# Kernel optimization log

Measured on AMD Instinct MI355X. Metric: run time of the kernel, lower is better.

## Reference

```python
import jax, jax.numpy as jnp
import numpy as np

VOCAB, EDIM, WFEAT, LABELS, SLOPE = 50000, 128, 128, 2, 0.01
N = 8192

def setup_inputs() -> dict:
    key = jax.random.key(0)
    ks = jax.random.split(key, 8)
    inSen = jax.random.randint(ks[0], (N,), 0, VOCAB, dtype=jnp.int64) if jax.config.read('jax_enable_x64') else jax.random.randint(ks[0], (N,), 0, VOCAB, dtype=jnp.int32)
    adj = jax.random.randint(ks[1], (N, N), 0, 2, dtype=jnp.int32)
    emb = jax.random.normal(ks[2], (VOCAB, EDIM), dtype=jnp.float32)
    W = jax.random.normal(ks[3], (EDIM, WFEAT), dtype=jnp.float32) * (1.0 / np.sqrt(EDIM))
    a_src = jax.random.normal(ks[4], (WFEAT,), dtype=jnp.float32) * (1.0 / np.sqrt(WFEAT))
    a_dst = jax.random.normal(ks[5], (WFEAT,), dtype=jnp.float32) * (1.0 / np.sqrt(WFEAT))
    cls_W = jax.random.normal(ks[6], (WFEAT, LABELS), dtype=jnp.float32) * (1.0 / np.sqrt(WFEAT))
    cls_b = jax.random.normal(ks[7], (LABELS,), dtype=jnp.float32) * 0.01
    return {"inSen": inSen, "adj": adj, "selfLink": 1, "emb": emb, "W": W,
            "a_src": a_src, "a_dst": a_dst, "cls_W": cls_W, "cls_b": cls_b}

def reference(inSen, adj, selfLink, emb, W, a_src, a_dst, cls_W, cls_b):
    # Embedding lookup: (N, edim)
    words = emb[inSen]
    # GAT layer: linear projection then adjacency-masked additive attention
    h = words @ W                              # (N, wFeat)
    f_src = h @ a_src                          # (N,)
    f_dst = h @ a_dst                          # (N,)
    e = jax.nn.leaky_relu(f_src[:, None] + f_dst[None, :], negative_slope=SLOPE)  # (N, N)
    mask = (adj + selfLink * jnp.eye(adj.shape[0], dtype=adj.dtype)) > 0
    e = jnp.where(mask, e, jnp.float32(-1e9))
    attention = jax.nn.softmax(e, axis=1)      # (N, N)
    sentence = attention @ h                   # (N, wFeat)
    # Max pool over words, classify
    poolSentence = jnp.max(sentence, axis=0)   # (wFeat,)
    label = jax.nn.softmax(poolSentence @ cls_W + cls_b, axis=0)  # (labels,)
    return (poolSentence, attention, sentence, label)
```

## Files before the change

### kernel.cpp

```cpp
#include <hip/hip_runtime.h>
#include <hip/hip_bf16.h>

#define NR 8192
#define WF 128
#define MSTRIDE 260

typedef short bf16x8 __attribute__((ext_vector_type(8)));
typedef float f32x4 __attribute__((ext_vector_type(4)));
typedef int   i32x4 __attribute__((ext_vector_type(4)));

static __device__ __forceinline__ unsigned int f2bf(float f) {
    unsigned int u = __float_as_uint(f);
    return (u + 0x7fffu + ((u >> 16) & 1u)) >> 16;
}
static __device__ __forceinline__ void atomicMaxF(float* addr, float v) {
    if (v >= 0.f) atomicMax((int*)addr, __float_as_int(v));
    else          atomicMin((unsigned int*)addr, __float_as_uint(v));
}
static __device__ __forceinline__ float lrelu(float x) { return x > 0.f ? x : 0.01f * x; }

__global__ __launch_bounds__(256) void k_proj(
    const int* __restrict__ inSen, const float* __restrict__ emb,
    const float* __restrict__ W, const float* __restrict__ a_src,
    const float* __restrict__ a_dst, float* __restrict__ f_src,
    float* __restrict__ f_dst, float* __restrict__ maxfd,
    unsigned short* __restrict__ hB)
{
    __shared__ float ht[16 * 132];
    const int t = threadIdx.x;
    const int f = t & 127, rh = t >> 7;
    const int i0 = blockIdx.x * 16;

    int wd[8];
    #pragma unroll
    for (int r = 0; r < 8; ++r) wd[r] = inSen[i0 + rh * 8 + r];
    float h[8];
    #pragma unroll
    for (int r = 0; r < 8; ++r) h[r] = 0.f;

    for (int k4 = 0; k4 < 32; ++k4) {
        const float w0 = W[(k4 * 4 + 0) * WF + f];
        const float w1 = W[(k4 * 4 + 1) * WF + f];
        const float w2 = W[(k4 * 4 + 2) * WF + f];
        const float w3 = W[(k4 * 4 + 3) * WF + f];
        #pragma unroll
        for (int r = 0; r < 8; ++r) {
            float4 ev = ((const float4*)(emb + (size_t)wd[r] * 128))[k4];
            h[r] += ev.x * w0 + ev.y * w1 + ev.z * w2 + ev.w * w3;
        }
    }
    #pragma unroll
    for (int r = 0; r < 8; ++r) ht[(rh * 8 + r) * 132 + f] = h[r];
    __syncthreads();

    if (t < 16) {
        float s = 0.f, d = 0.f;
        for (int k4 = 0; k4 < 32; ++k4) {
            float4 hv = *(const float4*)(ht + t * 132 + k4 * 4);
            float4 as = ((const float4*)a_src)[k4];
            float4 ad = ((const float4*)a_dst)[k4];
            s += hv.x * as.x + hv.y * as.y + hv.z * as.z + hv.w * as.w;
            d += hv.x * ad.x + hv.y * ad.y + hv.z * ad.z + hv.w * ad.w;
        }
        f_src[i0 + t] = s;
        f_dst[i0 + t] = d;
        float dm = d;
        #pragma unroll
        for (int o = 1; o < 16; o <<= 1) dm = fmaxf(dm, __shfl_xor(dm, o));
        if (t == 0) atomicMaxF(maxfd, dm);
    }
    {
        const int kb = blockIdx.x >> 1, half = blockIdx.x & 1;
        const int nf = t >> 5, l32 = t & 31;
        const int qloc = l32 >> 4, fx = l32 & 15;
        const int lane = (half * 2 + qloc) * 16 + fx;
        const float* hp = ht + (qloc * 8) * 132 + nf * 16 + fx;
        uint4 v;
        v.x = f2bf(hp[0 * 132]) | (f2bf(hp[1 * 132]) << 16);
        v.y = f2bf(hp[2 * 132]) | (f2bf(hp[3 * 132]) << 16);
        v.z = f2bf(hp[4 * 132]) | (f2bf(hp[5 * 132]) << 16);
        v.w = f2bf(hp[6 * 132]) | (f2bf(hp[7 * 132]) << 16);
        *(uint4*)(hB + ((size_t)kb * 8 + nf) * 512 + lane * 8) = v;
    }
}

static __device__ __forceinline__ void adj_chunk(
    int c, i32x4 a, const float* __restrict__ fdl, int lane, int row, int sl,
    float fs, float C, int shl,
    unsigned int* __restrict__ mrow, float& sum)
{
    const float4 f = *(const float4*)(fdl + c * 256 + 4 * lane);
    const bool m0 = a[0] > 0, m1 = a[1] > 0, m2 = a[2] > 0, m3 = a[3] > 0;
    float p0 = m0 ? __expf(lrelu(fs + f.x) - C) : 0.f;
    float p1 = m1 ? __expf(lrelu(fs + f.y) - C) : 0.f;
    float p2 = m2 ? __expf(lrelu(fs + f.z) - C) : 0.f;
    float p3 = m3 ? __expf(lrelu(fs + f.w) - C) : 0.f;
    unsigned int nib = (m0 ? 1u : 0u) | (m1 ? 2u : 0u) | (m2 ? 4u : 0u) | (m3 ? 8u : 0u);
    float ssum = p0 + p1 + p2 + p3;
    if (c == (row >> 8)) {
        if (lane == ((row & 255) >> 2)) {
            const int jd = row & 3;
            const int aj = jd == 0 ? a[0] : jd == 1 ? a[1] : jd == 2 ? a[2] : a[3];
            const float fj = jd == 0 ? f.x : jd == 1 ? f.y : jd == 2 ? f.z : f.w;
            const bool mo = aj > 0, mn = (aj + sl) > 0;
            if (mn != mo) {
                const float pd = __expf(lrelu(fs + fj) - C);
                if (mn) { nib |= 1u << jd; ssum += pd; }
                else    { nib &= ~(1u << jd); ssum -= pd; }
            }
        }
    }
    sum += ssum;
    unsigned int v = nib << shl;
    v |= __shfl_xor(v, 1);
    v |= __shfl_xor(v, 2);
    v |= __shfl_xor(v, 4);
    if ((lane & 7) == 0) mrow[c * 8 + (lane >> 3)] = v;
}

#define NTL(p) __builtin_nontemporal_load((const i32x4*)(p))

static __device__ __forceinline__ float adj_row(
    const int* __restrict__ ap, const float* __restrict__ fdl,
    int lane, int row, int sl, float fs, float C, int shl,
    unsigned int* __restrict__ mrow,
    i32x4 a0, i32x4 a1, i32x4 a2, i32x4 a3, i32x4 a4, i32x4 a5, i32x4 a6, i32x4 a7)
{
    float sum = 0.f;
    #define ADJC(c, reg) adj_chunk((c), (reg), fdl, lane, row, sl, fs, C, shl, mrow, sum)
    #pragma unroll 1
    for (int g = 0; g < 24; g += 8) {
        ADJC(g + 0, a0); a0 = NTL(ap + (g +  8) * 256);
        ADJC(g + 1, a1); a1 = NTL(ap + (g +  9) * 256);
        ADJC(g + 2, a2); a2 = NTL(ap + (g + 10) * 256);
        ADJC(g + 3, a3); a3 = NTL(ap + (g + 11) * 256);
        ADJC(g + 4, a4); a4 = NTL(ap + (g + 12) * 256);
        ADJC(g + 5, a5); a5 = NTL(ap + (g + 13) * 256);
        ADJC(g + 6, a6); a6 = NTL(ap + (g + 14) * 256);
        ADJC(g + 7, a7); a7 = NTL(ap + (g + 15) * 256);
    }
    ADJC(24, a0); ADJC(25, a1); ADJC(26, a2); ADJC(27, a3);
    ADJC(28, a4); ADJC(29, a5); ADJC(30, a6); ADJC(31, a7);
    #undef ADJC
    return sum;
}

__global__ __launch_bounds__(1024, 4) void k_fused(
    const int* __restrict__ adj, const int* __restrict__ slP,
    const float* __restrict__ f_src, const float* __restrict__ f_dst,
    const float* __restrict__ maxfd, const unsigned short* __restrict__ hB,
    float* __restrict__ att, float* __restrict__ sent, float* __restrict__ partial)
{
    __shared__ float fdl[NR];
    __shared__ __align__(16) unsigned int mask[32 * MSTRIDE];
    __shared__ float sums[32];
    const int t = threadIdx.x, lane = t & 63, w = t >> 6;
    const int i0 = blockIdx.x * 32;

    const int rowA = i0 + 2 * w;
    const int* __restrict__ apA = adj + (size_t)rowA * NR + 4 * lane;
    i32x4 a0 = NTL(apA + 0 * 256);
    i32x4 a1 = NTL(apA + 1 * 256);
    i32x4 a2 = NTL(apA + 2 * 256);
    i32x4 a3 = NTL(apA + 3 * 256);
    i32x4 a4 = NTL(apA + 4 * 256);
    i32x4 a5 = NTL(apA + 5 * 256);
    i32x4 a6 = NTL(apA + 6 * 256);
    i32x4 a7 = NTL(apA + 7 * 256);

    #pragma unroll
    for (int i = 0; i < 2; ++i)
        *(float4*)(fdl + (i * 1024 + t) * 4) = *(const float4*)(f_dst + (i * 1024 + t) * 4);

    const int sl = slP[0];
    const float mfd = maxfd[0];
    const int shl = 4 * (lane & 7);
    __syncthreads();

    {
        const float fsA = f_src[rowA];
        const float CA = lrelu(fsA + mfd);
        float s = adj_row(apA, fdl, lane, rowA, sl, fsA, CA, shl,
                          mask + (2 * w) * MSTRIDE, a0, a1, a2, a3, a4, a5, a6, a7);
        #pragma unroll
        for (int o = 1; o < 64; o <<= 1) s += __shfl_xor(s, o);
        if (lane == 0) sums[2 * w] = 1.0f / s;
    }
    {
        const int rowB = rowA + 1;
        const int* __restrict__ apB = adj + (size_t)rowB * NR + 4 * lane;
        i32x4 b0 = NTL(apB + 0 * 256);
        i32x4 b1 = NTL(apB + 1 * 256);
        i32x4 b2 = NTL(apB + 2 * 256);
        i32x4 b3 = NTL(apB + 3 * 256);
        i32x4 b4 = NTL(apB + 4 * 256);
        i32x4 b5 = NTL(apB + 5 * 256);
        i32x4 b6 = NTL(apB + 6 * 256);
        i32x4 b7 = NTL(apB + 7 * 256);
        const float fsB = f_src[rowB];
        const float CB = lrelu(fsB + mfd);
        float s = adj_row(apB, fdl, lane, rowB, sl, fsB, CB, shl,
                          mask + (2 * w + 1) * MSTRIDE, b0, b1, b2, b3, b4, b5, b6, b7);
        #pragma unroll
        for (int o = 1; o < 64; o <<= 1) s += __shfl_xor(s, o);
        if (lane == 0) sums[2 * w + 1] = 1.0f / s;
    }
    __syncthreads();

    const int ss = w >> 3, wk = w & 7;
    const int fx = lane & 15, quad = lane >> 4;
    const int lrow = ss * 16 + fx;
    const int row = i0 + lrow;
    const float fs = f_src[row];
    const float C = lrelu(fs + mfd);
    const float il = sums[lrow];
    float* __restrict__ ar = att + (size_t)row * NR;
    const unsigned int* __restrict__ mrow = mask + lrow * MSTRIDE;
    f32x4 acc[8] = {};
    const int k0 = wk * 1024;

    for (int kk4 = k0; kk4 < k0 + 1024; kk4 += 128) {
        const uint4 mw = *(const uint4*)(mrow + (kk4 >> 5));
        const unsigned int mwa[4] = {mw.x, mw.y, mw.z, mw.w};
        #pragma unroll
        for (int j4 = 0; j4 < 4; ++j4) {
            const int kk = kk4 + j4 * 32;
            const int kb = kk >> 5;
            const unsigned short* hp = hB + (size_t)kb * 4096 + lane * 8;
            bf16x8 bfr[8];
            #pragma unroll
            for (int nf = 0; nf < 8; ++nf) bfr[nf] = *(const bf16x8*)(hp + nf * 512);

            const unsigned int mbyte = (mwa[j4] >> (quad * 8)) & 0xffu;
            const float4 fd0 = *(const float4*)(fdl + kk + quad * 8);
            const float4 fd1 = *(const float4*)(fdl + kk + quad * 8 + 4);
            const float fv[8] = {fd0.x, fd0.y, fd0.z, fd0.w, fd1.x, fd1.y, fd1.z, fd1.w};
            float p[8];
            #pragma unroll
            for (int j = 0; j < 8; ++j)
                p[j] = ((mbyte >> j) & 1u) ? __expf(lrelu(fs + fv[j]) - C) : 0.f;

            const float4 w0 = make_float4(p[0] * il, p[1] * il, p[2] * il, p[3] * il);
            const float4 w1 = make_float4(p[4] * il, p[5] * il, p[6] * il, p[7] * il);
            *(float4*)(ar + kk + quad * 8) = w0;
            *(float4*)(ar + kk + quad * 8 + 4) = w1;

            union { uint4 u; bf16x8 v; } cv;
            cv.u.x = f2bf(p[0]) | (f2bf(p[1]) << 16);
            cv.u.y = f2bf(p[2]) | (f2bf(p[3]) << 16);
            cv.u.z = f2bf(p[4]) | (f2bf(p[5]) << 16);
            cv.u.w = f2bf(p[6]) | (f2bf(p[7]) << 16);
            #pragma unroll
            for (int nf = 0; nf < 8; ++nf)
                acc[nf] = __builtin_amdgcn_mfma_f32_16x16x32_bf16(cv.v, bfr[nf], acc[nf], 0, 0, 0);
        }
    }
    __syncthreads();
    float* tile = (float*)mask;
    *(float4*)(tile + t * 4) = make_float4(0.f, 0.f, 0.f, 0.f);
    __syncthreads();
    #pragma unroll
    for (int reg = 0; reg < 4; ++reg) {
        #pragma unroll
        for (int nf = 0; nf < 8; ++nf)
            atomicAdd(&tile[ss * 2048 + (quad * 4 + reg) * 128 + nf * 16 + fx], acc[nf][reg]);
    }
    __syncthreads();
    {
        const int e = t * 4;
        const int st2 = e >> 11, off = e & 2047, r = off >> 7, f0 = off & 127;
        const float vin = sums[st2 * 16 + r];
        float4 vv = make_float4(tile[e] * vin, tile[e + 1] * vin,
                                tile[e + 2] * vin, tile[e + 3] * vin);
        *(float4*)(sent + (size_t)(i0 + st2 * 16 + r) * WF + f0) = vv;
    }
    if (t < 128) {
        float mx = -1e30f;
        #pragma unroll
        for (int s = 0; s < 2; ++s)
            for (int r = 0; r < 16; ++r)
                mx = fmaxf(mx, tile[s * 2048 + r * 128 + t] * sums[s * 16 + r]);
        partial[blockIdx.x * 128 + t] = mx;
    }
}

__global__ __launch_bounds__(128) void k_label(
    const float* __restrict__ partial, const float* __restrict__ cls_W,
    const float* __restrict__ cls_b, float* __restrict__ pool,
    float* __restrict__ label)
{
    __shared__ float s0[128], s1[128];
    const int t = threadIdx.x;
    float m0 = -1e30f, m1 = -1e30f, m2 = -1e30f, m3 = -1e30f;
    for (int b = 0; b < 256; b += 4) {
        m0 = fmaxf(m0, partial[(b + 0) * 128 + t]);
        m1 = fmaxf(m1, partial[(b + 1) * 128 + t]);
        m2 = fmaxf(m2, partial[(b + 2) * 128 + t]);
        m3 = fmaxf(m3, partial[(b + 3) * 128 + t]);
    }
    const float m = fmaxf(fmaxf(m0, m1), fmaxf(m2, m3));
    pool[t] = m;
    s0[t] = m * cls_W[t * 2 + 0];
    s1[t] = m * cls_W[t * 2 + 1];
    __syncthreads();
    if (t == 0) {
        float z0 = cls_b[0], z1 = cls_b[1];
        for (int f = 0; f < 128; ++f) { z0 += s0[f]; z1 += s1[f]; }
        float mm = fmaxf(z0, z1);
        float e0 = __expf(z0 - mm), e1 = __expf(z1 - mm);
        float inv = 1.0f / (e0 + e1);
        label[0] = e0 * inv;
        label[1] = e1 * inv;
    }
}

extern "C" void kernel_launch(void* const* d_in, const int* in_sizes, int n_in,
                              void* d_out, int out_size, void* d_ws, size_t ws_size,
                              hipStream_t stream)
{
    const int*   inSen    = (const int*)d_in[0];
    const int*   adj      = (const int*)d_in[1];
    const int*   selfLink = (const int*)d_in[2];
    const float* emb      = (const float*)d_in[3];
    const float* W        = (const float*)d_in[4];
    const float* a_src    = (const float*)d_in[5];
    const float* a_dst    = (const float*)d_in[6];
    const float* cls_W    = (const float*)d_in[7];
    const float* cls_b    = (const float*)d_in[8];

    float* out   = (float*)d_out;
    float* pool  = out;
    float* att   = out + 128;
    float* sent  = att + (size_t)NR * NR;
    float* label = sent + (size_t)NR * WF;

    char* ws = (char*)d_ws;
    unsigned short* hB    = (unsigned short*)ws;
    float* f_src   = (float*)(ws + (2u << 20));
    float* f_dst   = f_src + NR;
    float* maxfd   = f_dst + NR;
    float* partial = maxfd + 64;

    hipMemsetAsync(maxfd, 0xFF, 4, stream);
    k_proj<<<NR / 16, 256, 0, stream>>>(inSen, emb, W, a_src, a_dst, f_src, f_dst, maxfd, hB);
    k_fused<<<NR / 32, 1024, 0, stream>>>(adj, selfLink, f_src, f_dst, maxfd, hB, att, sent, partial);
    k_label<<<1, 128, 0, stream>>>(partial, cls_W, cls_b, pool, label);
}
```

Before: 591.6 us.

## Interleave two adjacency rows in mask pass and batch attention stores

The adjacency-scan phase now processes rows A and B of each wave together, prefetching 4 chunks per row in parallel instead of 8 chunks for one row then the other. This keeps more independent loads in flight across both rows and removes the serial second-row startup latency. The attention pass pairs two 32-column steps, defers the global attention stores until after both MFMA groups, and uses the bf16x2 conversion intrinsic instead of a manual rounding routine. The trade is higher register pressure and shallower per-row prefetch depth.

```diff
diff --git a/kernel.cpp b/kernel.cpp
--- a/kernel.cpp
+++ b/kernel.cpp
@@ -120,31 +120,6 @@
 
 #define NTL(p) __builtin_nontemporal_load((const i32x4*)(p))
 
-static __device__ __forceinline__ float adj_row(
-    const int* __restrict__ ap, const float* __restrict__ fdl,
-    int lane, int row, int sl, float fs, float C, int shl,
-    unsigned int* __restrict__ mrow,
-    i32x4 a0, i32x4 a1, i32x4 a2, i32x4 a3, i32x4 a4, i32x4 a5, i32x4 a6, i32x4 a7)
-{
-    float sum = 0.f;
-    #define ADJC(c, reg) adj_chunk((c), (reg), fdl, lane, row, sl, fs, C, shl, mrow, sum)
-    #pragma unroll 1
-    for (int g = 0; g < 24; g += 8) {
-        ADJC(g + 0, a0); a0 = NTL(ap + (g +  8) * 256);
-        ADJC(g + 1, a1); a1 = NTL(ap + (g +  9) * 256);
-        ADJC(g + 2, a2); a2 = NTL(ap + (g + 10) * 256);
-        ADJC(g + 3, a3); a3 = NTL(ap + (g + 11) * 256);
-        ADJC(g + 4, a4); a4 = NTL(ap + (g + 12) * 256);
-        ADJC(g + 5, a5); a5 = NTL(ap + (g + 13) * 256);
-        ADJC(g + 6, a6); a6 = NTL(ap + (g + 14) * 256);
-        ADJC(g + 7, a7); a7 = NTL(ap + (g + 15) * 256);
-    }
-    ADJC(24, a0); ADJC(25, a1); ADJC(26, a2); ADJC(27, a3);
-    ADJC(28, a4); ADJC(29, a5); ADJC(30, a6); ADJC(31, a7);
-    #undef ADJC
-    return sum;
-}
-
 __global__ __launch_bounds__(1024, 4) void k_fused(
     const int* __restrict__ adj, const int* __restrict__ slP,
     const float* __restrict__ f_src, const float* __restrict__ f_dst,
@@ -157,16 +132,17 @@
     const int t = threadIdx.x, lane = t & 63, w = t >> 6;
     const int i0 = blockIdx.x * 32;
 
-    const int rowA = i0 + 2 * w;
+    const int rowA = i0 + 2 * w, rowB = rowA + 1;
     const int* __restrict__ apA = adj + (size_t)rowA * NR + 4 * lane;
-    i32x4 a0 = NTL(apA + 0 * 256);
-    i32x4 a1 = NTL(apA + 1 * 256);
-    i32x4 a2 = NTL(apA + 2 * 256);
-    i32x4 a3 = NTL(apA + 3 * 256);
-    i32x4 a4 = NTL(apA + 4 * 256);
-    i32x4 a5 = NTL(apA + 5 * 256);
-    i32x4 a6 = NTL(apA + 6 * 256);
-    i32x4 a7 = NTL(apA + 7 * 256);
+    const int* __restrict__ apB = adj + (size_t)rowB * NR + 4 * lane;
+    i32x4 A0 = NTL(apA + 0 * 256);
+    i32x4 A1 = NTL(apA + 1 * 256);
+    i32x4 A2 = NTL(apA + 2 * 256);
+    i32x4 A3 = NTL(apA + 3 * 256);
+    i32x4 B0 = NTL(apB + 0 * 256);
+    i32x4 B1 = NTL(apB + 1 * 256);
+    i32x4 B2 = NTL(apB + 2 * 256);
+    i32x4 B3 = NTL(apB + 3 * 256);
 
     #pragma unroll
     for (int i = 0; i < 2; ++i)
@@ -178,32 +154,36 @@
     __syncthreads();
 
     {
-        const float fsA = f_src[rowA];
-        const float CA = lrelu(fsA + mfd);
-        float s = adj_row(apA, fdl, lane, rowA, sl, fsA, CA, shl,
-                          mask + (2 * w) * MSTRIDE, a0, a1, a2, a3, a4, a5, a6, a7);
-        #pragma unroll
-        for (int o = 1; o < 64; o <<= 1) s += __shfl_xor(s, o);
-        if (lane == 0) sums[2 * w] = 1.0f / s;
-    }
-    {
-        const int rowB = rowA + 1;
-        const int* __restrict__ apB = adj + (size_t)rowB * NR + 4 * lane;
-        i32x4 b0 = NTL(apB + 0 * 256);
-        i32x4 b1 = NTL(apB + 1 * 256);
-        i32x4 b2 = NTL(apB + 2 * 256);
-        i32x4 b3 = NTL(apB + 3 * 256);
-        i32x4 b4 = NTL(apB + 4 * 256);
-        i32x4 b5 = NTL(apB + 5 * 256);
-        i32x4 b6 = NTL(apB + 6 * 256);
-        i32x4 b7 = NTL(apB + 7 * 256);
-        const float fsB = f_src[rowB];
-        const float CB = lrelu(fsB + mfd);
-        float s = adj_row(apB, fdl, lane, rowB, sl, fsB, CB, shl,
-                          mask + (2 * w + 1) * MSTRIDE, b0, b1, b2, b3, b4, b5, b6, b7);
-        #pragma unroll
-        for (int o = 1; o < 64; o <<= 1) s += __shfl_xor(s, o);
-        if (lane == 0) sums[2 * w + 1] = 1.0f / s;
+        const float fsA = f_src[rowA], CA = lrelu(fsA + mfd);
+        const float fsB = f_src[rowB], CB = lrelu(fsB + mfd);
+        unsigned int* __restrict__ mrA = mask + (2 * w) * MSTRIDE;
+        unsigned int* __restrict__ mrB = mask + (2 * w + 1) * MSTRIDE;
+        float sA = 0.f, sB = 0.f;
+        #define ADJA(c, reg) adj_chunk((c), (reg), fdl, lane, rowA, sl, fsA, CA, shl, mrA, sA)
+        #define ADJB(c, reg) adj_chunk((c), (reg), fdl, lane, rowB, sl, fsB, CB, shl, mrB, sB)
+        #pragma unroll 1
+        for (int g = 0; g < 28; g += 4) {
+            ADJA(g + 0, A0); A0 = NTL(apA + (g + 4) * 256);
+            ADJB(g + 0, B0); B0 = NTL(apB + (g + 4) * 256);
+            ADJA(g + 1, A1); A1 = NTL(apA + (g + 5) * 256);
+            ADJB(g + 1, B1); B1 = NTL(apB + (g + 5) * 256);
+            ADJA(g + 2, A2); A2 = NTL(apA + (g + 6) * 256);
+            ADJB(g + 2, B2); B2 = NTL(apB + (g + 6) * 256);
+            ADJA(g + 3, A3); A3 = NTL(apA + (g + 7) * 256);
+            ADJB(g + 3, B3); B3 = NTL(apB + (g + 7) * 256);
+        }
+        ADJA(28, A0); ADJB(28, B0);
+        ADJA(29, A1); ADJB(29, B1);
+        ADJA(30, A2); ADJB(30, B2);
+        ADJA(31, A3); ADJB(31, B3);
+        #undef ADJA
+        #undef ADJB
+        #pragma unroll
+        for (int o = 1; o < 64; o <<= 1) {
+            sA += __shfl_xor(sA, o);
+            sB += __shfl_xor(sB, o);
+        }
+        if (lane == 0) { sums[2 * w] = 1.0f / sA; sums[2 * w + 1] = 1.0f / sB; }
     }
     __syncthreads();
 
@@ -223,36 +203,58 @@
         const uint4 mw = *(const uint4*)(mrow + (kk4 >> 5));
         const unsigned int mwa[4] = {mw.x, mw.y, mw.z, mw.w};
         #pragma unroll
-        for (int j4 = 0; j4 < 4; ++j4) {
-            const int kk = kk4 + j4 * 32;
-            const int kb = kk >> 5;
-            const unsigned short* hp = hB + (size_t)kb * 4096 + lane * 8;
-            bf16x8 bfr[8];
-            #pragma unroll
-            for (int nf = 0; nf < 8; ++nf) bfr[nf] = *(const bf16x8*)(hp + nf * 512);
-
-            const unsigned int mbyte = (mwa[j4] >> (quad * 8)) & 0xffu;
-            const float4 fd0 = *(const float4*)(fdl + kk + quad * 8);
-            const float4 fd1 = *(const float4*)(fdl + kk + quad * 8 + 4);
-            const float fv[8] = {fd0.x, fd0.y, fd0.z, fd0.w, fd1.x, fd1.y, fd1.z, fd1.w};
-            float p[8];
-            #pragma unroll
-            for (int j = 0; j < 8; ++j)
-                p[j] = ((mbyte >> j) & 1u) ? __expf(lrelu(fs + fv[j]) - C) : 0.f;
-
-            const float4 w0 = make_float4(p[0] * il, p[1] * il, p[2] * il, p[3] * il);
-            const float4 w1 = make_float4(p[4] * il, p[5] * il, p[6] * il, p[7] * il);
-            *(float4*)(ar + kk + quad * 8) = w0;
-            *(float4*)(ar + kk + quad * 8 + 4) = w1;
-
-            union { uint4 u; bf16x8 v; } cv;
-            cv.u.x = f2bf(p[0]) | (f2bf(p[1]) << 16);
-            cv.u.y = f2bf(p[2]) | (f2bf(p[3]) << 16);
-            cv.u.z = f2bf(p[4]) | (f2bf(p[5]) << 16);
-            cv.u.w = f2bf(p[6]) | (f2bf(p[7]) << 16);
-            #pragma unroll
-            for (int nf = 0; nf < 8; ++nf)
-                acc[nf] = __builtin_amdgcn_mfma_f32_16x16x32_bf16(cv.v, bfr[nf], acc[nf], 0, 0, 0);
+        for (int j2 = 0; j2 < 2; ++j2) {
+            const int kkA = kk4 + (2 * j2) * 32;
+            const int kkB = kkA + 32;
+            float pA[8], pB[8];
+            {
+                const unsigned short* hp = hB + (size_t)(kkA >> 5) * 4096 + lane * 8;
+                bf16x8 bfr[8];
+                #pragma unroll
+                for (int nf = 0; nf < 8; ++nf) bfr[nf] = *(const bf16x8*)(hp + nf * 512);
+                const unsigned int mbyte = (mwa[2 * j2] >> (quad * 8)) & 0xffu;
+                const float4 fd0 = *(const float4*)(fdl + kkA + quad * 8);
+                const float4 fd1 = *(const float4*)(fdl + kkA + quad * 8 + 4);
+                const float fv[8] = {fd0.x, fd0.y, fd0.z, fd0.w, fd1.x, fd1.y, fd1.z, fd1.w};
+                #pragma unroll
+                for (int j = 0; j < 8; ++j)
+                    pA[j] = ((mbyte >> j) & 1u) ? __expf(lrelu(fs + fv[j]) - C) : 0.f;
+                union { __hip_bfloat162 h2[4]; bf16x8 v; } cv;
+                #pragma unroll
+                for (int j = 0; j < 4; ++j)
+                    cv.h2[j] = __float22bfloat162_rn(make_float2(pA[2 * j], pA[2 * j + 1]));
+                #pragma unroll
+                for (int nf = 0; nf < 8; ++nf)
+                    acc[nf] = __builtin_amdgcn_mfma_f32_16x16x32_bf16(cv.v, bfr[nf], acc[nf], 0, 0, 0);
+            }
+            {
+                const unsigned short* hp = hB + (size_t)(kkB >> 5) * 4096 + lane * 8;
+                bf16x8 bfr[8];
+                #pragma unroll
+                for (int nf = 0; nf < 8; ++nf) bfr[nf] = *(const bf16x8*)(hp + nf * 512);
+                const unsigned int mbyte = (mwa[2 * j2 + 1] >> (quad * 8)) & 0xffu;
+                const float4 fd0 = *(const float4*)(fdl + kkB + quad * 8);
+                const float4 fd1 = *(const float4*)(fdl + kkB + quad * 8 + 4);
+                const float fv[8] = {fd0.x, fd0.y, fd0.z, fd0.w, fd1.x, fd1.y, fd1.z, fd1.w};
+                #pragma unroll
+                for (int j = 0; j < 8; ++j)
+                    pB[j] = ((mbyte >> j) & 1u) ? __expf(lrelu(fs + fv[j]) - C) : 0.f;
+                union { __hip_bfloat162 h2[4]; bf16x8 v; } cv;
+                #pragma unroll
+                for (int j = 0; j < 4; ++j)
+                    cv.h2[j] = __float22bfloat162_rn(make_float2(pB[2 * j], pB[2 * j + 1]));
+                #pragma unroll
+                for (int nf = 0; nf < 8; ++nf)
+                    acc[nf] = __builtin_amdgcn_mfma_f32_16x16x32_bf16(cv.v, bfr[nf], acc[nf], 0, 0, 0);
+            }
+            *(float4*)(ar + kkA + quad * 8) =
+                make_float4(pA[0] * il, pA[1] * il, pA[2] * il, pA[3] * il);
+            *(float4*)(ar + kkA + quad * 8 + 4) =
+                make_float4(pA[4] * il, pA[5] * il, pA[6] * il, pA[7] * il);
+            *(float4*)(ar + kkB + quad * 8) =
+                make_float4(pB[0] * il, pB[1] * il, pB[2] * il, pB[3] * il);
+            *(float4*)(ar + kkB + quad * 8 + 4) =
+                make_float4(pB[4] * il, pB[5] * il, pB[6] * il, pB[7] * il);
         }
     }
     __syncthreads();
```

New measurement: 595.4 us. No clear change (+0.7%).
